# Kernel optimization log

Hardware: AMD Instinct MI355X
Metric: run time of the kernel (lower is better)

The kernel has to match this reference:

```python
import jax, jax.numpy as jnp
import numpy as np
from jax import lax

SPAN = 11
K = 2 * SPAN + 1          # 23 -> 529 offsets
SIG_RGB = 0.1
SIG_XY = 6.0
LAM = 0.15
B, C, H, W = 2, 3, 160, 160


def _patches(x):
    """x: (N, C, H, W) -> (N, C, K, K, H, W), zero-padded.
    patch[di, dj] at pixel (i, j) equals x[i + di - SPAN, j + dj - SPAN],
    matching the torch module's shifted-slice double loop (dx = di - SPAN)."""
    n, c, h, w = x.shape
    xp = jnp.pad(x, ((0, 0), (0, 0), (SPAN, SPAN), (SPAN, SPAN)))

    def get(off):
        di = off // K
        dj = off % K
        return lax.dynamic_slice(xp, (0, 0, di, dj), (n, c, h, w))

    p = jax.vmap(get)(jnp.arange(K * K))              # (K*K, N, C, H, W)
    return p.reshape(K, K, n, c, h, w).transpose(2, 3, 0, 1, 4, 5)


def setup_inputs() -> dict:
    key = jax.random.key(0)
    k1, k2, k3, k4, k5 = jax.random.split(key, 5)
    logit = jax.random.normal(k1, (B, C, H, W), jnp.float32)
    target = jax.random.randint(k2, (B, H, W), 0, C)
    # small-magnitude image so exp(-0.5*(x - patch/0.1)^2) does not fully underflow
    image = jax.random.uniform(k3, (B, 3, H, W), jnp.float32) * 0.1
    source_map = (jax.random.uniform(k4, (B, 1, H, W)) > 0.5).astype(jnp.float32)
    destination_map = (jax.random.uniform(k5, (B, H, W)) > 0.5).astype(jnp.float32)
    return dict(logit=logit, target=target, image=image,
                source_map=source_map, destination_map=destination_map)


def _gcrf(image, y_hat, source_map, m_dst):
    b, c, h, w = y_hat.shape
    img_p = _patches(image)                                  # (B,3,K,K,H,W)
    valid = _patches(jnp.ones((1, 1, h, w), image.dtype))[0, 0]  # (K,K,H,W) in-bounds mask
    # NOTE: faithful to source bug: only the shifted feature is divided by sigma
    drgb = image[:, :, None, None] - img_p / SIG_RGB
    k_rgb = jnp.exp(-0.5 * jnp.sum(drgb * drgb, axis=1))     # (B,K,K,H,W)
    ii, jj = jnp.meshgrid(jnp.arange(h, dtype=image.dtype),
                          jnp.arange(w, dtype=image.dtype), indexing='ij')
    idx = jnp.stack([ii, jj])[None]                          # (1,2,H,W)
    idx_p = _patches(idx)[0]                                 # (2,K,K,H,W)
    dxy = idx[0][:, None, None] - idx_p / SIG_XY
    k_xy = jnp.exp(-0.5 * jnp.sum(dxy * dxy, axis=0))        # (K,K,H,W)
    kmat = (k_rgb + k_xy[None]) * valid[None]                # out-of-bounds offsets stay 0
    m_src = _patches(source_map)[:, 0]                       # (B,K,K,H,W)
    Kg = kmat * m_src * m_dst[:, None, None]                 # gated kernel
    U = _patches(y_hat)                                      # (B,C,K,K,H,W)
    Egy = jnp.einsum('bcijhw,bijhw->bchw', U, Kg)            # sum over window
    temp = jnp.einsum('bchw,bdhw->bcd', Egy, y_hat)          # (B,C,C)
    Moff = 1.0 - jnp.eye(c, dtype=y_hat.dtype)               # off-diagonal compatibility
    return jnp.sum(Moff * temp) / (b * h * w)


def reference(logit, target, image, source_map, destination_map):
    y_hat = jax.nn.softmax(logit, axis=1)
    m_dst = 1.0 - destination_map
    L_gcrf = _gcrf(image, y_hat, source_map, m_dst)
    logp = jax.nn.log_softmax(logit, axis=1)
    L_ce = -jnp.take_along_axis(logp, target[:, None], axis=1)[:, 0]  # (B,H,W)
    L_ce = jnp.mean(L_ce * destination_map)
    return L_ce + LAM * L_gcrf
```

## Files before the change

kernel.cpp:

```cpp
#include <hip/hip_runtime.h>

#define Bn 2
#define Cn 3
#define Hn 160
#define Wn 160
#define SPANc 11
#define Kc 23
#define HWn (Hn * Wn)
#define PW 182
#define PP (PW * PW)
#define LAMc 0.15f
#define INVN (1.0f / (float)(Bn * HWn))
#define TJ 32
#define Gc 4
#define TI 32
#define NROW (TI + Kc - 1)
#define NREC (NROW * TJ)
#define CEXP (-0.72134752f)
#define CX   (14.42695041f)
#define CA   (0.72134752f)
#define NPREP ((Bn * PP + 255) / 256)
#define NCELL 64
#define CELLSTRIDE 64

__device__ __forceinline__ float wave_reduce64(float v) {
#pragma unroll
    for (int off = 32; off > 0; off >>= 1) v += __shfl_down(v, off, 64);
    return v;
}

__device__ __forceinline__ unsigned int bf16pk(float a, float b) {
    unsigned int ua = __float_as_uint(a), ub = __float_as_uint(b);
    ua += 0x7fffu + ((ua >> 16) & 1u);
    ub += 0x7fffu + ((ub >> 16) & 1u);
    return (ua & 0xffff0000u) | (ub >> 16);
}

__global__ __launch_bounds__(256) void prep_kernel(
    const float* __restrict__ logit, const int* __restrict__ target,
    const float* __restrict__ image, const float* __restrict__ srcmap,
    const float* __restrict__ dstmap, uint4* __restrict__ gU4,
    float4* __restrict__ cvec, float* __restrict__ pc, float* __restrict__ cells)
{
    int idx = blockIdx.x * 256 + threadIdx.x;
    float ce = 0.0f;
    if (idx < NCELL) cells[idx * CELLSTRIDE] = 0.0f;
    if (idx < Bn * PP) {
        int b   = idx / PP;
        int rem = idx - b * PP;
        int ip  = rem / PW;
        int jp  = rem - ip * PW;
        int i = ip - SPANc, j = jp - SPANc;
        if ((unsigned)i < (unsigned)Hn && (unsigned)j < (unsigned)Wn) {
            int r = i * Wn + j;
            int p = b * HWn + r;
            const float* lg = logit + (size_t)b * Cn * HWn + r;
            float l0 = lg[0], l1 = lg[HWn], l2 = lg[2 * HWn];
            float m = fmaxf(l0, fmaxf(l1, l2));
            float e0 = __expf(l0 - m), e1 = __expf(l1 - m), e2 = __expf(l2 - m);
            float s = e0 + e1 + e2;
            float inv = 1.0f / s;
            float y0 = e0 * inv, y1 = e1 * inv, y2 = e2 * inv;
            float lse = m + __logf(s);

            const float* im = image + (size_t)b * 3 * HWn + r;
            float p0 = im[0], p1 = im[HWn], p2 = im[2 * HWn];
            float sv = srcmap[p];
            float dv = dstmap[p];

            float B = (p0 * p0 + p1 * p1 + p2 * p2) * (100.0f * CA);
            gU4[idx] = make_uint4(bf16pk(p0, p1), bf16pk(p2, -B),
                                  bf16pk(sv * y0, sv * y1), bf16pk(sv * y2, 0.0f));

            float md = LAMc * (1.0f - dv) * INVN;
            cvec[p] = make_float4(md * (1.0f - y0), md * (1.0f - y1),
                                  md * (1.0f - y2), 0.0f);

            int t = target[p];
            float lt = (t == 0) ? l0 : ((t == 1) ? l1 : l2);
            ce = (lse - lt) * dv * INVN;
        } else {
            gU4[idx] = make_uint4(0u, 0u, 0u, 0u);
        }
    }

    float v = wave_reduce64(ce);
    __shared__ float wsum[4];
    int tid = threadIdx.x;
    if ((tid & 63) == 0) wsum[tid >> 6] = v;
    __syncthreads();
    if (tid == 0) pc[blockIdx.x] = wsum[0] + wsum[1] + wsum[2] + wsum[3];
}

__device__ __forceinline__ void unpk(uint4 ru, float& p0, float& p1, float& p2,
                                     float& mB, float& q0, float& q1, float& q2) {
    p0 = __uint_as_float(ru.x & 0xffff0000u);
    p1 = __uint_as_float(ru.x << 16);
    p2 = __uint_as_float(ru.y & 0xffff0000u);
    mB = __uint_as_float(ru.y << 16);
    q0 = __uint_as_float(ru.z & 0xffff0000u);
    q1 = __uint_as_float(ru.z << 16);
    q2 = __uint_as_float(ru.w & 0xffff0000u);
}

template<bool XY>
__device__ __forceinline__ void tap(float p0, float p1, float p2, float mB,
                                    float q0, float q1, float q2,
                                    float c0s, float c1s, float c2s, float mA,
                                    bool xy_on, float dy2, float dxv,
                                    float& e0, float& e1, float& e2)
{
    float e = fmaf(c0s, p0, fmaf(c1s, p1, fmaf(c2s, p2, mB)));
    float k;
    if constexpr (XY) {
        k = __builtin_amdgcn_exp2f(e + mA);
        if (xy_on) k += __builtin_amdgcn_exp2f(fmaf(dxv, dxv, dy2) * CEXP);
    } else {
        k = __builtin_amdgcn_exp2f(e);
    }
    e0 = fmaf(k, q0, e0);
    e1 = fmaf(k, q1, e1);
    e2 = fmaf(k, q2, e2);
}

template<bool XY>
__device__ __forceinline__ void row_taps(uint4 ru, int r,
    const float* c0s, const float* c1s, const float* c2s, const float* mA,
    bool xy_on, float dy2, float fi0, float eg[Gc][3], int clo, int chi)
{
    float p0, p1, p2, mB, q0, q1, q2;
    unpk(ru, p0, p1, p2, mB, q0, q1, q2);
    float dxb = XY ? (fi0 - (fi0 + (float)(r - SPANc)) * (1.0f / 6.0f)) : 0.0f;
#pragma unroll
    for (int c = 0; c < Gc; ++c) {
        if (c < clo || c > chi) continue;
        tap<XY>(p0, p1, p2, mB, q0, q1, q2, c0s[c], c1s[c], c2s[c], mA[c],
                xy_on, dy2, dxb + (float)c, eg[c][0], eg[c][1], eg[c][2]);
    }
}

template<bool XY>
__device__ __forceinline__ void window_loop(
    const uint4* sU4, int lbase,
    const float* c0s, const float* c1s, const float* c2s, const float* mA,
    bool xy_on, float dy2, float fi0, float eg[Gc][3])
{
#pragma unroll
    for (int r = 0; r < 3; ++r) {
        row_taps<XY>(sU4[lbase + r * TJ], r, c0s, c1s, c2s, mA,
                     xy_on, dy2, fi0, eg, 0, r);
    }
#pragma unroll 2
    for (int r = 3; r <= 22; ++r) {
        row_taps<XY>(sU4[lbase + r * TJ], r, c0s, c1s, c2s, mA,
                     xy_on, dy2, fi0, eg, 0, 3);
    }
#pragma unroll
    for (int r = 23; r <= 25; ++r) {
        row_taps<XY>(sU4[lbase + r * TJ], r, c0s, c1s, c2s, mA,
                     xy_on, dy2, fi0, eg, r - 22, 3);
    }
}

__global__ __launch_bounds__(256, 5) void gcrf_kernel(
    const uint4* __restrict__ gU4, const float4* __restrict__ cvec,
    float* __restrict__ cells)
{
    __shared__ uint4 sU4[NREC];

    int tx = threadIdx.x;
    int ty = threadIdx.y;
    int tid = ty * TJ + tx;
    int jx = blockIdx.x;
    int j  = jx * TJ + tx;
    int by = blockIdx.y;
    int b  = by / 5;
    int it = by - b * 5;
    int i0g = it * TI + ty * Gc;
    int dj = blockIdx.z;

    size_t g0 = (size_t)b * PP + (size_t)(it * TI) * PW + (jx * TJ + dj);
    for (int n = tid; n < NREC; n += 256) {
        int rr = n >> 5, cc = n & 31;
        sU4[n] = gU4[g0 + (size_t)rr * PW + cc];
    }
    __syncthreads();

    bool isxy = (jx == 0 && it == 0);

    int lbase = ty * Gc * TJ + tx;
    float c0s[Gc], c1s[Gc], c2s[Gc], mA[Gc], kAe[Gc];
#pragma unroll
    for (int c = 0; c < Gc; ++c) {
        uint4 cu = sU4[lbase + (c + SPANc) * TJ];
        float cc0 = __uint_as_float(cu.x & 0xffff0000u);
        float cc1 = __uint_as_float(cu.x << 16);
        float cc2 = __uint_as_float(cu.y & 0xffff0000u);
        c0s[c] = cc0 * CX; c1s[c] = cc1 * CX; c2s[c] = cc2 * CX;
        mA[c] = -CA * fmaf(cc0, cc0, fmaf(cc1, cc1, cc2 * cc2));
        kAe[c] = isxy ? 1.0f : __builtin_amdgcn_exp2f(mA[c]);
    }

    bool xy_on = (j < 16) && (i0g < 16);
    float dy = (float)j - (float)(j + dj - SPANc) * (1.0f / 6.0f);
    float dy2 = dy * dy;
    float fi0 = (float)i0g;

    float eg[Gc][3];
#pragma unroll
    for (int c = 0; c < Gc; ++c) { eg[c][0] = 0.f; eg[c][1] = 0.f; eg[c][2] = 0.f; }

    if (isxy) {
        window_loop<true>(sU4, lbase, c0s, c1s, c2s, mA, xy_on, dy2, fi0, eg);
    } else {
        window_loop<false>(sU4, lbase, c0s, c1s, c2s, mA, false, dy2, fi0, eg);
    }

    const float4* cv = cvec + ((size_t)b * HWn + (size_t)i0g * Wn + j);
    float contrib = 0.0f;
#pragma unroll
    for (int c = 0; c < Gc; ++c) {
        float4 t = cv[(size_t)c * Wn];
        float d = eg[c][0] * t.x + eg[c][1] * t.y + eg[c][2] * t.z;
        contrib = fmaf(kAe[c], d, contrib);
    }

    float v = wave_reduce64(contrib);
    __shared__ float wsum[4];
    if ((tid & 63) == 0) wsum[tid >> 6] = v;
    __syncthreads();
    if (tid == 0) {
        int bflat = (blockIdx.z * gridDim.y + blockIdx.y) * gridDim.x + blockIdx.x;
        atomicAdd(cells + (size_t)(bflat & (NCELL - 1)) * CELLSTRIDE,
                  wsum[0] + wsum[1] + wsum[2] + wsum[3]);
    }
}

__global__ __launch_bounds__(64) void finalize_kernel(
    const float* __restrict__ cells, const float* __restrict__ pc,
    float* __restrict__ out)
{
    int t = threadIdx.x;
    float s = cells[(size_t)t * CELLSTRIDE];
    for (int k = t; k < NPREP; k += 64) s += pc[k];
    float v = wave_reduce64(s);
    if (t == 0) out[0] = v;
}

extern "C" void kernel_launch(void* const* d_in, const int* in_sizes, int n_in,
                              void* d_out, int out_size, void* d_ws, size_t ws_size,
                              hipStream_t stream)
{
    const float* logit  = (const float*)d_in[0];
    const int*   target = (const int*)d_in[1];
    const float* image  = (const float*)d_in[2];
    const float* srcmap = (const float*)d_in[3];
    const float* dstmap = (const float*)d_in[4];
    float* out = (float*)d_out;

    const size_t NRECG = (size_t)Bn * PP;
    float*  pc    = (float*)((char*)d_ws + 256);
    float*  cells = (float*)((char*)d_ws + 4096);
    uint4*  gU4   = (uint4*)((char*)d_ws + 4096 + 16384);
    float4* cvec  = (float4*)((char*)d_ws + 4096 + 16384 + NRECG * 16);

    prep_kernel<<<NPREP, 256, 0, stream>>>(logit, target, image, srcmap, dstmap,
                                           gU4, cvec, pc, cells);
    dim3 grid(Wn / TJ, (Hn / TI) * Bn, Kc);
    dim3 blk(TJ, 8);
    gcrf_kernel<<<grid, blk, 0, stream>>>(gU4, cvec, cells);
    finalize_kernel<<<1, 64, 0, stream>>>(cells, pc, out);
}
```

Baseline: 79.59 us.

## Fuse prep into gcrf kernel and replace atomics with per-block partials

Drops the separate prep kernel. Each gcrf block now computes softmax, the packed bf16 records and the CE terms on the fly from the raw inputs while filling shared memory, and the CE term is added only by blocks with dj==SPAN. Atomic cell accumulation is replaced with per-block partial sums that a single finalize block reduces. This removes one launch and the global round trip through the intermediate buffers, but every one of the 23 dj blocks covering a tile redoes the softmax and record packing, and 460 records plus gather loads are recomputed per block.

```diff
diff --git a/kernel.cpp b/kernel.cpp
--- a/kernel.cpp
+++ b/kernel.cpp
@@ -7,8 +7,6 @@
 #define SPANc 11
 #define Kc 23
 #define HWn (Hn * Wn)
-#define PW 182
-#define PP (PW * PW)
 #define LAMc 0.15f
 #define INVN (1.0f / (float)(Bn * HWn))
 #define TJ 32
@@ -19,9 +17,7 @@
 #define CEXP (-0.72134752f)
 #define CX   (14.42695041f)
 #define CA   (0.72134752f)
-#define NPREP ((Bn * PP + 255) / 256)
-#define NCELL 64
-#define CELLSTRIDE 64
+#define NBLK (5 * 10 * 23)
 
 __device__ __forceinline__ float wave_reduce64(float v) {
 #pragma unroll
@@ -34,62 +30,6 @@
     ua += 0x7fffu + ((ua >> 16) & 1u);
     ub += 0x7fffu + ((ub >> 16) & 1u);
     return (ua & 0xffff0000u) | (ub >> 16);
-}
-
-__global__ __launch_bounds__(256) void prep_kernel(
-    const float* __restrict__ logit, const int* __restrict__ target,
-    const float* __restrict__ image, const float* __restrict__ srcmap,
-    const float* __restrict__ dstmap, uint4* __restrict__ gU4,
-    float4* __restrict__ cvec, float* __restrict__ pc, float* __restrict__ cells)
-{
-    int idx = blockIdx.x * 256 + threadIdx.x;
-    float ce = 0.0f;
-    if (idx < NCELL) cells[idx * CELLSTRIDE] = 0.0f;
-    if (idx < Bn * PP) {
-        int b   = idx / PP;
-        int rem = idx - b * PP;
-        int ip  = rem / PW;
-        int jp  = rem - ip * PW;
-        int i = ip - SPANc, j = jp - SPANc;
-        if ((unsigned)i < (unsigned)Hn && (unsigned)j < (unsigned)Wn) {
-            int r = i * Wn + j;
-            int p = b * HWn + r;
-            const float* lg = logit + (size_t)b * Cn * HWn + r;
-            float l0 = lg[0], l1 = lg[HWn], l2 = lg[2 * HWn];
-            float m = fmaxf(l0, fmaxf(l1, l2));
-            float e0 = __expf(l0 - m), e1 = __expf(l1 - m), e2 = __expf(l2 - m);
-            float s = e0 + e1 + e2;
-            float inv = 1.0f / s;
-            float y0 = e0 * inv, y1 = e1 * inv, y2 = e2 * inv;
-            float lse = m + __logf(s);
-
-            const float* im = image + (size_t)b * 3 * HWn + r;
-            float p0 = im[0], p1 = im[HWn], p2 = im[2 * HWn];
-            float sv = srcmap[p];
-            float dv = dstmap[p];
-
-            float B = (p0 * p0 + p1 * p1 + p2 * p2) * (100.0f * CA);
-            gU4[idx] = make_uint4(bf16pk(p0, p1), bf16pk(p2, -B),
-                                  bf16pk(sv * y0, sv * y1), bf16pk(sv * y2, 0.0f));
-
-            float md = LAMc * (1.0f - dv) * INVN;
-            cvec[p] = make_float4(md * (1.0f - y0), md * (1.0f - y1),
-                                  md * (1.0f - y2), 0.0f);
-
-            int t = target[p];
-            float lt = (t == 0) ? l0 : ((t == 1) ? l1 : l2);
-            ce = (lse - lt) * dv * INVN;
-        } else {
-            gU4[idx] = make_uint4(0u, 0u, 0u, 0u);
-        }
-    }
-
-    float v = wave_reduce64(ce);
-    __shared__ float wsum[4];
-    int tid = threadIdx.x;
-    if ((tid & 63) == 0) wsum[tid >> 6] = v;
-    __syncthreads();
-    if (tid == 0) pc[blockIdx.x] = wsum[0] + wsum[1] + wsum[2] + wsum[3];
 }
 
 __device__ __forceinline__ void unpk(uint4 ru, float& p0, float& p1, float& p2,
@@ -163,8 +103,9 @@
 }
 
 __global__ __launch_bounds__(256, 5) void gcrf_kernel(
-    const uint4* __restrict__ gU4, const float4* __restrict__ cvec,
-    float* __restrict__ cells)
+    const float* __restrict__ logit, const int* __restrict__ target,
+    const float* __restrict__ image, const float* __restrict__ srcmap,
+    const float* __restrict__ dstmap, float* __restrict__ partial)
 {
     __shared__ uint4 sU4[NREC];
 
@@ -179,14 +120,35 @@
     int i0g = it * TI + ty * Gc;
     int dj = blockIdx.z;
 
-    size_t g0 = (size_t)b * PP + (size_t)(it * TI) * PW + (jx * TJ + dj);
+    int i_top  = it * TI - SPANc;
+    int j_left = jx * TJ + dj - SPANc;
     for (int n = tid; n < NREC; n += 256) {
         int rr = n >> 5, cc = n & 31;
-        sU4[n] = gU4[g0 + (size_t)rr * PW + cc];
+        int ii = i_top + rr, jj = j_left + cc;
+        uint4 rec = make_uint4(0u, 0u, 0u, 0u);
+        if ((unsigned)ii < (unsigned)Hn && (unsigned)jj < (unsigned)Wn) {
+            int r = ii * Wn + jj;
+            int p = b * HWn + r;
+            const float* lg = logit + (size_t)b * Cn * HWn + r;
+            float l0 = lg[0], l1 = lg[HWn], l2 = lg[2 * HWn];
+            float m = fmaxf(l0, fmaxf(l1, l2));
+            float e0 = __expf(l0 - m), e1 = __expf(l1 - m), e2 = __expf(l2 - m);
+            float s = e0 + e1 + e2;
+            float inv = 1.0f / s;
+            float y0 = e0 * inv, y1 = e1 * inv, y2 = e2 * inv;
+            const float* im = image + (size_t)b * 3 * HWn + r;
+            float p0 = im[0], p1 = im[HWn], p2 = im[2 * HWn];
+            float sv = srcmap[p];
+            float Bv = (p0 * p0 + p1 * p1 + p2 * p2) * (100.0f * CA);
+            rec = make_uint4(bf16pk(p0, p1), bf16pk(p2, -Bv),
+                             bf16pk(sv * y0, sv * y1), bf16pk(sv * y2, 0.0f));
+        }
+        sU4[n] = rec;
     }
     __syncthreads();
 
     bool isxy = (jx == 0 && it == 0);
+    bool ceb  = (dj == SPANc);
 
     int lbase = ty * Gc * TJ + tx;
     float c0s[Gc], c1s[Gc], c2s[Gc], mA[Gc], kAe[Gc];
@@ -216,13 +178,29 @@
         window_loop<false>(sU4, lbase, c0s, c1s, c2s, mA, false, dy2, fi0, eg);
     }
 
-    const float4* cv = cvec + ((size_t)b * HWn + (size_t)i0g * Wn + j);
     float contrib = 0.0f;
 #pragma unroll
     for (int c = 0; c < Gc; ++c) {
-        float4 t = cv[(size_t)c * Wn];
-        float d = eg[c][0] * t.x + eg[c][1] * t.y + eg[c][2] * t.z;
+        int r = (i0g + c) * Wn + j;
+        int p = b * HWn + r;
+        const float* lg = logit + (size_t)b * Cn * HWn + r;
+        float l0 = lg[0], l1 = lg[HWn], l2 = lg[2 * HWn];
+        float m = fmaxf(l0, fmaxf(l1, l2));
+        float e0 = __expf(l0 - m), e1 = __expf(l1 - m), e2 = __expf(l2 - m);
+        float s = e0 + e1 + e2;
+        float inv = 1.0f / s;
+        float y0 = e0 * inv, y1 = e1 * inv, y2 = e2 * inv;
+        float dv = dstmap[p];
+        float md = LAMc * (1.0f - dv) * INVN;
+        float t0 = md * (1.0f - y0), t1 = md * (1.0f - y1), t2 = md * (1.0f - y2);
+        float d = eg[c][0] * t0 + eg[c][1] * t1 + eg[c][2] * t2;
         contrib = fmaf(kAe[c], d, contrib);
+        if (ceb) {
+            float lse = m + __logf(s);
+            int t = target[p];
+            float lt = (t == 0) ? l0 : ((t == 1) ? l1 : l2);
+            contrib += (lse - lt) * dv * INVN;
+        }
     }
 
     float v = wave_reduce64(contrib);
@@ -231,20 +209,21 @@
     __syncthreads();
     if (tid == 0) {
         int bflat = (blockIdx.z * gridDim.y + blockIdx.y) * gridDim.x + blockIdx.x;
-        atomicAdd(cells + (size_t)(bflat & (NCELL - 1)) * CELLSTRIDE,
-                  wsum[0] + wsum[1] + wsum[2] + wsum[3]);
-    }
-}
-
-__global__ __launch_bounds__(64) void finalize_kernel(
-    const float* __restrict__ cells, const float* __restrict__ pc,
-    float* __restrict__ out)
-{
-    int t = threadIdx.x;
-    float s = cells[(size_t)t * CELLSTRIDE];
-    for (int k = t; k < NPREP; k += 64) s += pc[k];
+        partial[bflat] = wsum[0] + wsum[1] + wsum[2] + wsum[3];
+    }
+}
+
+__global__ __launch_bounds__(256) void finalize_kernel(
+    const float* __restrict__ partial, float* __restrict__ out)
+{
+    int tid = threadIdx.x;
+    float s = 0.0f;
+    for (int k = tid; k < NBLK; k += 256) s += partial[k];
     float v = wave_reduce64(s);
-    if (t == 0) out[0] = v;
+    __shared__ float wsum[4];
+    if ((tid & 63) == 0) wsum[tid >> 6] = v;
+    __syncthreads();
+    if (tid == 0) out[0] = wsum[0] + wsum[1] + wsum[2] + wsum[3];
 }
 
 extern "C" void kernel_launch(void* const* d_in, const int* in_sizes, int n_in,
@@ -258,16 +237,11 @@
     const float* dstmap = (const float*)d_in[4];
     float* out = (float*)d_out;
 
-    const size_t NRECG = (size_t)Bn * PP;
-    float*  pc    = (float*)((char*)d_ws + 256);
-    float*  cells = (float*)((char*)d_ws + 4096);
-    uint4*  gU4   = (uint4*)((char*)d_ws + 4096 + 16384);
-    float4* cvec  = (float4*)((char*)d_ws + 4096 + 16384 + NRECG * 16);
-
-    prep_kernel<<<NPREP, 256, 0, stream>>>(logit, target, image, srcmap, dstmap,
-                                           gU4, cvec, pc, cells);
+    float* partial = (float*)((char*)d_ws + 4096);
+
     dim3 grid(Wn / TJ, (Hn / TI) * Bn, Kc);
     dim3 blk(TJ, 8);
-    gcrf_kernel<<<grid, blk, 0, stream>>>(gU4, cvec, cells);
-    finalize_kernel<<<1, 64, 0, stream>>>(cells, pc, out);
-}
+    gcrf_kernel<<<grid, blk, 0, stream>>>(logit, target, image, srcmap, dstmap,
+                                          partial);
+    finalize_kernel<<<1, 256, 0, stream>>>(partial, out);
+}
```

New measurement: 80.89 us. Within noise of the previous version (+1.6%).
